# Kernel optimization log

Measured on AMD Instinct MI355X. Metric: run time of the kernel, lower is better.

The kernel has to match this reference:

```python
import jax, jax.numpy as jnp
import numpy as np

C_IN = 256
C_OUT = 256
NUM_HEADS = 4
C_HEAD = C_OUT // NUM_HEADS  # 64
ALPHA = 0.2
NEG_FILL = -9e15


def setup_inputs() -> dict:
    key = jax.random.key(0)
    k1, k2, k3, k4, k5 = jax.random.split(key, 5)
    B, N = 1, 4096
    node_feats = jax.random.normal(k1, (B, N, C_IN), dtype=jnp.float32)
    adj_matrix = jax.random.randint(k2, (B, N, N), 0, 2, dtype=jnp.int32)
    # xavier_uniform with gain=1.414 on projection weight (fan_in=C_IN, fan_out=C_OUT)
    lim_w = 1.414 * np.sqrt(6.0 / (C_IN + C_OUT))
    W = jax.random.uniform(k3, (C_IN, C_OUT), dtype=jnp.float32, minval=-lim_w, maxval=lim_w)
    b = jnp.zeros((C_OUT,), dtype=jnp.float32)
    lim_a = 1.414 * np.sqrt(6.0 / (NUM_HEADS + 2 * C_HEAD))
    a = jax.random.uniform(k4, (NUM_HEADS, 2 * C_HEAD), dtype=jnp.float32, minval=-lim_a, maxval=lim_a)
    return {"node_feats": node_feats, "adj_matrix": adj_matrix, "W": W, "b": b, "a": a}


def reference(node_feats, adj_matrix, W, b, a):
    B, N, _ = node_feats.shape
    # linear projection -> (B, N, H, C_HEAD)
    feats = (node_feats @ W + b).reshape(B, N, NUM_HEADS, C_HEAD)
    # attention logit for edge (i -> j): a_src . h_i + a_dst . h_j, per head
    a_src, a_dst = a[:, :C_HEAD], a[:, C_HEAD:]
    src = jnp.einsum('bnhc,hc->bnh', feats, a_src)  # indexed by row i
    dst = jnp.einsum('bnhc,hc->bnh', feats, a_dst)  # indexed by col j
    logits = src[:, :, None, :] + dst[:, None, :, :]  # (B, N, N, H)
    logits = jnp.where(logits >= 0, logits, ALPHA * logits)  # LeakyReLU(0.2)
    attn = jnp.where(adj_matrix[..., None] == 1, logits, NEG_FILL)
    probs = jax.nn.softmax(attn, axis=2)  # softmax over source nodes j
    out = jnp.einsum('bijh,bjhc->bihc', probs, feats)
    return out.reshape(B, N, NUM_HEADS * C_HEAD)  # concat heads
```

## Files before the change

### kernel.cpp

```cpp
#include <hip/hip_runtime.h>

#define NN 4096
#define C 256
#define NH 4
#define CH 64
#define JSPLIT 8
#define JSLICE (NN / JSPLIT)
#define NJT (JSLICE / 32)

typedef float f32x4 __attribute__((ext_vector_type(4)));
typedef __bf16 b16x8 __attribute__((ext_vector_type(8)));
typedef unsigned short u16x8 __attribute__((ext_vector_type(8)));
typedef unsigned int u32x4 __attribute__((ext_vector_type(4)));

__device__ inline float fast_exp2(float x) {
#if __has_builtin(__builtin_amdgcn_exp2f)
  return __builtin_amdgcn_exp2f(x);
#else
  return exp2f(x);
#endif
}

__device__ inline unsigned pack2bf(float f0, float f1) {
  unsigned u0 = __float_as_uint(f0) + 0x8000u;
  unsigned u1 = __float_as_uint(f1) + 0x8000u;
  return __builtin_amdgcn_perm(u1, u0, 0x07060302u);
}

__global__ __launch_bounds__(256) void k_prep(
    const float* __restrict__ X, const float* __restrict__ W,
    unsigned short* __restrict__ Xbf, unsigned short* __restrict__ WT) {
  const int b = blockIdx.x, t = threadIdx.x;
  if (b < 1024) {
    const int idx = b * 256 + t;
    const float4 v = ((const float4*)X)[idx];
    uint2 st;
    st.x = pack2bf(v.x, v.y);
    st.y = pack2bf(v.z, v.w);
    ((uint2*)Xbf)[idx] = st;
  } else {
    const int c = b - 1024;
    const float w = W[(size_t)t * C + c];
    WT[(size_t)c * C + t] = (unsigned short)((__float_as_uint(w) + 0x8000u) >> 16);
  }
}

__global__ __launch_bounds__(256) void k_feats(
    const unsigned short* __restrict__ Xbf, const unsigned short* __restrict__ WT,
    const float* __restrict__ bias, const float* __restrict__ av,
    unsigned short* __restrict__ F, float2* __restrict__ srcAB,
    float2* __restrict__ EdT2) {
  const int i0 = blockIdx.x * 16;
  const int h = threadIdx.x >> 6;
  const int lane = threadIdx.x & 63;
  const int q = lane >> 4, n = lane & 15;
  const int c0 = h * CH;
  const float LOG2E = 1.4426950408889634f;

  const f32x4 zero = {0.f, 0.f, 0.f, 0.f};
  f32x4 acc[4];
#pragma unroll
  for (int g = 0; g < 4; ++g) acc[g] = zero;

  const unsigned short* ap = Xbf + (size_t)(i0 + n) * C + q * 8;
#pragma unroll
  for (int kt = 0; kt < 8; ++kt) {
    const b16x8 aF = __builtin_bit_cast(b16x8, *(const u16x8*)(ap + kt * 32));
#pragma unroll
    for (int g = 0; g < 4; ++g) {
      const b16x8 bF = __builtin_bit_cast(b16x8,
          *(const u16x8*)(WT + (size_t)(c0 + g * 16 + n) * C + kt * 32 + q * 8));
      acc[g] = __builtin_amdgcn_mfma_f32_16x16x32_bf16(aF, bF, acc[g], 0, 0, 0);
    }
  }

  float fb[4][4], asv[4], adv[4];
#pragma unroll
  for (int g = 0; g < 4; ++g) {
    const float bs = bias[c0 + g * 16 + n];
    asv[g] = av[h * 128 + g * 16 + n];
    adv[g] = av[h * 128 + 64 + g * 16 + n];
#pragma unroll
    for (int r = 0; r < 4; ++r) fb[g][r] = acc[g][r] + bs;
  }
  const int jt = i0 >> 5, half = (i0 >> 4) & 1;
  const int qp = half * 2 + (q >> 1);
#pragma unroll
  for (int g = 0; g < 4; ++g) {
    uint2 st;
    st.x = pack2bf(fb[g][0], fb[g][1]);
    st.y = pack2bf(fb[g][2], fb[g][3]);
    *(uint2*)(F + ((size_t)((jt * NH + h) * 4 + g)) * 512 + (qp * 16 + n) * 8 + 4 * (q & 1)) = st;
  }
#pragma unroll
  for (int r = 0; r < 4; ++r) {
    float p = 0.f, d = 0.f;
#pragma unroll
    for (int g = 0; g < 4; ++g) {
      p = fmaf(fb[g][r], asv[g], p);
      d = fmaf(fb[g][r], adv[g], d);
    }
#pragma unroll
    for (int m = 1; m < 16; m <<= 1) {
      p += __shfl_xor(p, m);
      d += __shfl_xor(d, m);
    }
    if (n == 0) {
      const int row = i0 + q * 4 + r;
      const float dL = d * LOG2E;
      EdT2[(size_t)h * NN + row] = make_float2(fast_exp2(dL), fast_exp2(0.2f * dL));
      const float x = p + 16.0f;
      const float m2 = fmaxf(x, 0.2f * x) * LOG2E;
      srcAB[(size_t)row * NH + h] = make_float2(
          fast_exp2(fmaf(p, LOG2E, -m2)),
          fast_exp2(fmaf(0.2f * p, LOG2E, -m2)));
    }
  }
}

__global__ __launch_bounds__(256, 4) void k_attn(
    const int* __restrict__ adj,
    const unsigned short* __restrict__ F,
    const float2* __restrict__ srcAB, const float2* __restrict__ EdT2,
    _Float16* __restrict__ pacc, float* __restrict__ lpart) {
  const int slice = blockIdx.x;
  const int i0 = blockIdx.y * 32;
  const int h = threadIdx.x >> 6;
  const int lane = threadIdx.x & 63;
  const int q = lane >> 4, n = lane & 15;
  const int jbase = slice * JSLICE;

  const int r0 = i0 + n, r1 = i0 + 16 + n;
  const float2 ab0 = srcAB[(size_t)r0 * NH + h];
  const float2 ab1 = srcAB[(size_t)r1 * NH + h];

  const f32x4 zero = {0.f, 0.f, 0.f, 0.f};
  f32x4 acc0[4], acc1[4], lacc0 = zero, lacc1 = zero;
#pragma unroll
  for (int g = 0; g < 4; ++g) { acc0[g] = zero; acc1[g] = zero; }

  u16x8 ou;
#pragma unroll
  for (int jj = 0; jj < 8; ++jj) ou[jj] = 0x3F80;
  const b16x8 ones = __builtin_bit_cast(b16x8, ou);

  const int* aj0 = adj + (size_t)r0 * NN + jbase + q * 8;
  const int* aj1 = adj + (size_t)r1 * NN + jbase + q * 8;
  const float* dp2 = (const float*)(EdT2 + (size_t)h * NN + jbase);
  const unsigned short* fp = F + ((size_t)((jbase >> 5) * NH + h) * 4) * 512 + lane * 8;

#pragma unroll
  for (int a = 0; a < 4; ++a) {
#pragma unroll
    for (int b = 0; b < 4; ++b) {
      const int jt = a * 4 + b;
      b16x8 bF[4];
#pragma unroll
      for (int g = 0; g < 4; ++g)
        bF[g] = __builtin_bit_cast(b16x8,
            *(const u16x8*)(fp + (size_t)(jt * NH * 4 + g) * 512));

      const int4 M0a = *(const int4*)(aj0 + jt * 32);
      const int4 M0b = *(const int4*)(aj0 + jt * 32 + 4);
      const int4 M1a = *(const int4*)(aj1 + jt * 32);
      const int4 M1b = *(const int4*)(aj1 + jt * 32 + 4);
      const int m0[8] = {M0a.x, M0a.y, M0a.z, M0a.w, M0b.x, M0b.y, M0b.z, M0b.w};
      const int m1[8] = {M1a.x, M1a.y, M1a.z, M1a.w, M1b.x, M1b.y, M1b.z, M1b.w};

      const float* dq = dp2 + jt * 64 + q * 16;
      const float4 dd0 = *(const float4*)(dq);
      const float4 dd1 = *(const float4*)(dq + 4);
      const float4 dd2 = *(const float4*)(dq + 8);
      const float4 dd3 = *(const float4*)(dq + 12);
      const float4 dd[4] = {dd0, dd1, dd2, dd3};

      u32x4 pk0, pk1;
#pragma unroll
      for (int k = 0; k < 4; ++k) {
        const float4 d = dd[k];
        const float e00 = m0[2 * k]     ? fmaxf(d.x * ab0.x, d.y * ab0.y) : 0.f;
        const float e01 = m0[2 * k + 1] ? fmaxf(d.z * ab0.x, d.w * ab0.y) : 0.f;
        const float e10 = m1[2 * k]     ? fmaxf(d.x * ab1.x, d.y * ab1.y) : 0.f;
        const float e11 = m1[2 * k + 1] ? fmaxf(d.z * ab1.x, d.w * ab1.y) : 0.f;
        pk0[k] = pack2bf(e00, e01);
        pk1[k] = pack2bf(e10, e11);
      }
      const b16x8 E0 = __builtin_bit_cast(b16x8, pk0);
      const b16x8 E1 = __builtin_bit_cast(b16x8, pk1);
#pragma unroll
      for (int g = 0; g < 4; ++g) {
        acc0[g] = __builtin_amdgcn_mfma_f32_16x16x32_bf16(E0, bF[g], acc0[g], 0, 0, 0);
        acc1[g] = __builtin_amdgcn_mfma_f32_16x16x32_bf16(E1, bF[g], acc1[g], 0, 0, 0);
      }
      lacc0 = __builtin_amdgcn_mfma_f32_16x16x32_bf16(E0, ones, lacc0, 0, 0, 0);
      lacc1 = __builtin_amdgcn_mfma_f32_16x16x32_bf16(E1, ones, lacc1, 0, 0, 0);
    }
  }

#pragma unroll
  for (int g = 0; g < 4; ++g)
#pragma unroll
    for (int r = 0; r < 4; ++r) {
      const int col = h * CH + g * 16 + n;
      pacc[((size_t)slice * NN + i0 + q * 4 + r) * C + col] = (_Float16)acc0[g][r];
      pacc[((size_t)slice * NN + i0 + 16 + q * 4 + r) * C + col] = (_Float16)acc1[g][r];
    }
  if (n == 0) {
#pragma unroll
    for (int r = 0; r < 4; ++r) {
      lpart[((size_t)slice * NN + i0 + q * 4 + r) * NH + h] = lacc0[r];
      lpart[((size_t)slice * NN + i0 + 16 + q * 4 + r) * NH + h] = lacc1[r];
    }
  }
}

__global__ __launch_bounds__(256) void k_final(
    const _Float16* __restrict__ pacc, const float* __restrict__ lpart,
    float* __restrict__ out) {
  const int i = blockIdx.x;
  const int c = threadIdx.x;
  const int h = c >> 6;
  float l = 0.f, sa = 0.f;
#pragma unroll
  for (int sp = 0; sp < JSPLIT; ++sp) {
    l += lpart[((size_t)sp * NN + i) * NH + h];
    sa += (float)pacc[((size_t)sp * NN + i) * C + c];
  }
  out[(size_t)i * C + c] = sa / l;
}

extern "C" void kernel_launch(void* const* d_in, const int* in_sizes, int n_in,
                              void* d_out, int out_size, void* d_ws, size_t ws_size,
                              hipStream_t stream) {
  const float* nf   = (const float*)d_in[0];
  const int* adj    = (const int*)d_in[1];
  const float* W    = (const float*)d_in[2];
  const float* bias = (const float*)d_in[3];
  const float* av   = (const float*)d_in[4];
  float* out = (float*)d_out;

  char* ws = (char*)d_ws;
  unsigned short* Xbf = (unsigned short*)ws;
  unsigned short* WT  = (unsigned short*)(ws + (2u << 20));
  unsigned short* F   = (unsigned short*)(ws + (2u << 20) + (128u << 10));
  float2* srcAB = (float2*)(ws + (4u << 20) + (128u << 10));
  float2* EdT2  = (float2*)(ws + (4u << 20) + (256u << 10));
  float* lpart  = (float*)(ws + (4u << 20) + (384u << 10));
  _Float16* pacc = (_Float16*)(ws + (8u << 20));

  k_prep<<<1280, 256, 0, stream>>>(nf, W, Xbf, WT);
  k_feats<<<NN / 16, 256, 0, stream>>>(Xbf, WT, bias, av, F, srcAB, EdT2);
  dim3 g2(JSPLIT, NN / 32);
  k_attn<<<g2, 256, 0, stream>>>(adj, F, srcAB, EdT2, pacc, lpart);
  k_final<<<NN, 256, 0, stream>>>(pacc, lpart, out);
}
```

Baseline: 160.3 us.

## Pre-pack adjacency into bitmask and double the attention j-split

A new stage in the prep kernel streams the int32 adjacency matrix once and packs it into a 1-bit-per-edge mask. The attention kernel then loads a few bytes per row and pulls mask bits out with lane shuffles instead of issuing wide int4 loads inside the MFMA loop. JSPLIT rises from 8 to 16, so each attention block covers half as many columns and the grid has twice as many blocks. In exchange, the partial-accumulator buffer and the final reduction both double in size, and the full 64MB adjacency read still happens, now in a separate kernel.

```diff
diff --git a/kernel.cpp b/kernel.cpp
--- a/kernel.cpp
+++ b/kernel.cpp
@@ -4,7 +4,7 @@
 #define C 256
 #define NH 4
 #define CH 64
-#define JSPLIT 8
+#define JSPLIT 16
 #define JSLICE (NN / JSPLIT)
 #define NJT (JSLICE / 32)
 
@@ -28,18 +28,29 @@
 }
 
 __global__ __launch_bounds__(256) void k_prep(
-    const float* __restrict__ X, const float* __restrict__ W,
+    const int* __restrict__ adj, const float* __restrict__ X,
+    const float* __restrict__ W, unsigned char* __restrict__ packed,
     unsigned short* __restrict__ Xbf, unsigned short* __restrict__ WT) {
   const int b = blockIdx.x, t = threadIdx.x;
-  if (b < 1024) {
+  if (b < 8192) {
     const int idx = b * 256 + t;
+    const int4 a0 = *(const int4*)(adj + (size_t)idx * 8);
+    const int4 a1 = *(const int4*)(adj + (size_t)idx * 8 + 4);
+    unsigned m = 0;
+    m |= (a0.x != 0) ? 1u : 0u;   m |= (a0.y != 0) ? 2u : 0u;
+    m |= (a0.z != 0) ? 4u : 0u;   m |= (a0.w != 0) ? 8u : 0u;
+    m |= (a1.x != 0) ? 16u : 0u;  m |= (a1.y != 0) ? 32u : 0u;
+    m |= (a1.z != 0) ? 64u : 0u;  m |= (a1.w != 0) ? 128u : 0u;
+    packed[idx] = (unsigned char)m;
+  } else if (b < 9216) {
+    const int idx = (b - 8192) * 256 + t;
     const float4 v = ((const float4*)X)[idx];
     uint2 st;
     st.x = pack2bf(v.x, v.y);
     st.y = pack2bf(v.z, v.w);
     ((uint2*)Xbf)[idx] = st;
   } else {
-    const int c = b - 1024;
+    const int c = b - 9216;
     const float w = W[(size_t)t * C + c];
     WT[(size_t)c * C + t] = (unsigned short)((__float_as_uint(w) + 0x8000u) >> 16);
   }
@@ -119,7 +130,7 @@
 }
 
 __global__ __launch_bounds__(256, 4) void k_attn(
-    const int* __restrict__ adj,
+    const unsigned char* __restrict__ packed,
     const unsigned short* __restrict__ F,
     const float2* __restrict__ srcAB, const float2* __restrict__ EdT2,
     _Float16* __restrict__ pacc, float* __restrict__ lpart) {
@@ -144,28 +155,27 @@
   for (int jj = 0; jj < 8; ++jj) ou[jj] = 0x3F80;
   const b16x8 ones = __builtin_bit_cast(b16x8, ou);
 
-  const int* aj0 = adj + (size_t)r0 * NN + jbase + q * 8;
-  const int* aj1 = adj + (size_t)r1 * NN + jbase + q * 8;
+  const uint2 m20 = *(const uint2*)(packed + (size_t)r0 * 512 + (jbase >> 3) + q * 8);
+  const uint2 m21 = *(const uint2*)(packed + (size_t)r1 * 512 + (jbase >> 3) + q * 8);
+
   const float* dp2 = (const float*)(EdT2 + (size_t)h * NN + jbase);
   const unsigned short* fp = F + ((size_t)((jbase >> 5) * NH + h) * 4) * 512 + lane * 8;
 
 #pragma unroll
   for (int a = 0; a < 4; ++a) {
 #pragma unroll
-    for (int b = 0; b < 4; ++b) {
-      const int jt = a * 4 + b;
+    for (int b = 0; b < 2; ++b) {
+      const int jt = a * 2 + b;
       b16x8 bF[4];
 #pragma unroll
       for (int g = 0; g < 4; ++g)
         bF[g] = __builtin_bit_cast(b16x8,
             *(const u16x8*)(fp + (size_t)(jt * NH * 4 + g) * 512));
 
-      const int4 M0a = *(const int4*)(aj0 + jt * 32);
-      const int4 M0b = *(const int4*)(aj0 + jt * 32 + 4);
-      const int4 M1a = *(const int4*)(aj1 + jt * 32);
-      const int4 M1b = *(const int4*)(aj1 + jt * 32 + 4);
-      const int m0[8] = {M0a.x, M0a.y, M0a.z, M0a.w, M0b.x, M0b.y, M0b.z, M0b.w};
-      const int m1[8] = {M1a.x, M1a.y, M1a.z, M1a.w, M1b.x, M1b.y, M1b.z, M1b.w};
+      const int w0 = b ? (int)m20.y : (int)m20.x;
+      const int w1 = b ? (int)m21.y : (int)m21.x;
+      const unsigned Mb0 = (unsigned(__shfl(w0, a * 16 + n)) >> (q * 8)) & 0xffu;
+      const unsigned Mb1 = (unsigned(__shfl(w1, a * 16 + n)) >> (q * 8)) & 0xffu;
 
       const float* dq = dp2 + jt * 64 + q * 16;
       const float4 dd0 = *(const float4*)(dq);
@@ -178,10 +188,10 @@
 #pragma unroll
       for (int k = 0; k < 4; ++k) {
         const float4 d = dd[k];
-        const float e00 = m0[2 * k]     ? fmaxf(d.x * ab0.x, d.y * ab0.y) : 0.f;
-        const float e01 = m0[2 * k + 1] ? fmaxf(d.z * ab0.x, d.w * ab0.y) : 0.f;
-        const float e10 = m1[2 * k]     ? fmaxf(d.x * ab1.x, d.y * ab1.y) : 0.f;
-        const float e11 = m1[2 * k + 1] ? fmaxf(d.z * ab1.x, d.w * ab1.y) : 0.f;
+        const float e00 = (Mb0 & (1u << (2 * k))) ? fmaxf(d.x * ab0.x, d.y * ab0.y) : 0.f;
+        const float e01 = (Mb0 & (2u << (2 * k))) ? fmaxf(d.z * ab0.x, d.w * ab0.y) : 0.f;
+        const float e10 = (Mb1 & (1u << (2 * k))) ? fmaxf(d.x * ab1.x, d.y * ab1.y) : 0.f;
+        const float e11 = (Mb1 & (2u << (2 * k))) ? fmaxf(d.z * ab1.x, d.w * ab1.y) : 0.f;
         pk0[k] = pack2bf(e00, e01);
         pk1[k] = pack2bf(e10, e11);
       }
@@ -240,17 +250,18 @@
   float* out = (float*)d_out;
 
   char* ws = (char*)d_ws;
-  unsigned short* Xbf = (unsigned short*)ws;
-  unsigned short* WT  = (unsigned short*)(ws + (2u << 20));
-  unsigned short* F   = (unsigned short*)(ws + (2u << 20) + (128u << 10));
-  float2* srcAB = (float2*)(ws + (4u << 20) + (128u << 10));
-  float2* EdT2  = (float2*)(ws + (4u << 20) + (256u << 10));
-  float* lpart  = (float*)(ws + (4u << 20) + (384u << 10));
+  unsigned char* packed  = (unsigned char*)ws;
+  unsigned short* Xbf    = (unsigned short*)(ws + (2u << 20));
+  unsigned short* WT     = (unsigned short*)(ws + (4u << 20));
+  unsigned short* F      = (unsigned short*)(ws + (4u << 20) + (256u << 10));
+  float2* srcAB = (float2*)(ws + (6u << 20) + (256u << 10));
+  float2* EdT2  = (float2*)(ws + (6u << 20) + (384u << 10));
+  float* lpart  = (float*)(ws + (6u << 20) + (512u << 10));
   _Float16* pacc = (_Float16*)(ws + (8u << 20));
 
-  k_prep<<<1280, 256, 0, stream>>>(nf, W, Xbf, WT);
+  k_prep<<<9472, 256, 0, stream>>>(adj, nf, W, packed, Xbf, WT);
   k_feats<<<NN / 16, 256, 0, stream>>>(Xbf, WT, bias, av, F, srcAB, EdT2);
   dim3 g2(JSPLIT, NN / 32);
-  k_attn<<<g2, 256, 0, stream>>>(adj, F, srcAB, EdT2, pacc, lpart);
+  k_attn<<<g2, 256, 0, stream>>>(packed, F, srcAB, EdT2, pacc, lpart);
   k_final<<<NN, 256, 0, stream>>>(pacc, lpart, out);
 }
```

After: 145.7 us. 1.1x faster.
